# Kernel optimization log

Hardware: AMD Instinct MI355X
Metric: run time of the kernel (lower is better)

Reference implementation:

```python
import jax, jax.numpy as jnp
import numpy as np

N_NODES = 50000
N_EDGES = 1600000
D_FEAT = 32


def setup_inputs() -> dict:
    key = jax.random.key(0)
    k1, k2, k3, k4 = jax.random.split(key, 4)
    node_feat = jax.random.normal(k1, (N_NODES, D_FEAT), dtype=jnp.float32)
    edge_feat = jax.random.normal(k2, (N_EDGES, D_FEAT), dtype=jnp.float32)
    eps = jnp.zeros((1,), dtype=jnp.float32)  # learnable eps, init 0
    src = jax.random.randint(k3, (N_EDGES,), 0, N_NODES, dtype=jnp.int64)
    dst = jax.random.randint(k4, (N_EDGES,), 0, N_NODES, dtype=jnp.int64)
    return {"node_feat": node_feat, "edge_feat": edge_feat, "eps": eps,
            "src": src, "dst": dst}


def reference(node_feat, edge_feat, eps, src, dst):
    # message: relu(h_src + h_edge) per edge  [E, D]
    m = jax.nn.relu(node_feat[src] + edge_feat)
    # sum-aggregate messages into destination nodes  [N, D]
    neigh = jax.ops.segment_sum(m, dst, num_segments=node_feat.shape[0])
    # eps-scaled residual
    return (1.0 + eps[0]) * node_feat + neigh
```

## Files before the change

kernel.cpp:

```cpp
#include <hip/hip_runtime.h>

#define N_NODES 50000
#define N_EDGES 1600000
#define D_FEAT 32
#define SCAN_BLOCK 1024
#define N_SCAN_BLOCKS ((N_NODES + SCAN_BLOCK - 1) / SCAN_BLOCK)

#define WS_CNT   0
#define WS_EXCL  (N_NODES)
#define WS_OFF   (2 * N_NODES)
#define WS_BSUM  (3 * N_NODES)
#define WS_BSUMX (3 * N_NODES + 64)
#define WS_RANK  (3 * N_NODES + 128)
#define WS_MSG   (3 * N_NODES + 128 + N_EDGES)


__global__ void hist_rank(const int* __restrict__ dst,
                          int* __restrict__ cnt,
                          int* __restrict__ rank) {
    int e = blockIdx.x * blockDim.x + threadIdx.x;
    if (e < N_EDGES) rank[e] = atomicAdd(&cnt[dst[e]], 1);
}

__global__ void scan_blocks(const int* __restrict__ cnt,
                            int* __restrict__ excl,
                            int* __restrict__ bsum) {
    __shared__ int lds[SCAN_BLOCK];
    int tid = threadIdx.x;
    int i = blockIdx.x * SCAN_BLOCK + tid;
    int v = (i < N_NODES) ? cnt[i] : 0;
    int sum = v;
    lds[tid] = v;
    __syncthreads();
    for (int ofs = 1; ofs < SCAN_BLOCK; ofs <<= 1) {
        int t = (tid >= ofs) ? lds[tid - ofs] : 0;
        __syncthreads();
        sum += t;
        lds[tid] = sum;
        __syncthreads();
    }
    if (i < N_NODES) excl[i] = sum - v;
    if (tid == SCAN_BLOCK - 1) bsum[blockIdx.x] = lds[SCAN_BLOCK - 1];
}

__global__ void scan_bsums(const int* __restrict__ bsum, int* __restrict__ bsumx) {
    int lane = threadIdx.x;
    int orig = (lane < N_SCAN_BLOCKS) ? bsum[lane] : 0;
    int v = orig;
    for (int o = 1; o < 64; o <<= 1) {
        int t = __shfl_up(v, o);
        if (lane >= o) v += t;
    }
    if (lane < N_SCAN_BLOCKS) bsumx[lane] = v - orig;
}

__global__ void finalize_off(const int* __restrict__ excl,
                             const int* __restrict__ bsumx,
                             int* __restrict__ off) {
    int i = blockIdx.x * SCAN_BLOCK + threadIdx.x;
    if (i < N_NODES) off[i] = excl[i] + bsumx[blockIdx.x];
}

__global__ void build_msg(const float* __restrict__ node_feat,
                          const float* __restrict__ edge_feat,
                          const int* __restrict__ src,
                          const int* __restrict__ dst,
                          const int* __restrict__ off,
                          const int* __restrict__ rank,
                          float* __restrict__ msg) {
    int t = blockIdx.x * blockDim.x + threadIdx.x;
    int e = t >> 3;
    int g = t & 7;
    if (e >= N_EDGES) return;

    int d = dst[e];
    int pos = off[d] + rank[e];
    int s = src[e];

    float4 ef = ((const float4*)edge_feat)[(size_t)e * 8 + g];
    float4 nf = ((const float4*)node_feat)[s * 8 + g];
    float4 m;
    m.x = fmaxf(nf.x + ef.x, 0.f);
    m.y = fmaxf(nf.y + ef.y, 0.f);
    m.z = fmaxf(nf.z + ef.z, 0.f);
    m.w = fmaxf(nf.w + ef.w, 0.f);
    ((float4*)msg)[(size_t)pos * 8 + g] = m;
}

__global__ void reduce_msgs(const float* __restrict__ node_feat,
                            const float* __restrict__ eps,
                            const int* __restrict__ off,
                            const int* __restrict__ cnt,
                            const float* __restrict__ msg,
                            float* __restrict__ out) {
    int t = blockIdx.x * blockDim.x + threadIdx.x;
    int n = t >> 3;
    int g = t & 7;
    if (n >= N_NODES) return;

    int start = off[n];
    int c = cnt[n];

    float4 acc = make_float4(0.f, 0.f, 0.f, 0.f);
    for (int i = 0; i < c; ++i) {
        float4 m = ((const float4*)msg)[(size_t)(start + i) * 8 + g];
        acc.x += m.x; acc.y += m.y; acc.z += m.z; acc.w += m.w;
    }

    float scale = 1.0f + eps[0];
    float4 h = ((const float4*)node_feat)[n * 8 + g];
    float4 o;
    o.x = scale * h.x + acc.x;
    o.y = scale * h.y + acc.y;
    o.z = scale * h.z + acc.z;
    o.w = scale * h.w + acc.w;
    ((float4*)out)[n * 8 + g] = o;
}


__global__ void fb_init_out(const float* __restrict__ node_feat,
                            const float* __restrict__ eps,
                            float* __restrict__ out) {
    int i = blockIdx.x * blockDim.x + threadIdx.x;
    const int n4 = N_NODES * D_FEAT / 4;
    float scale = 1.0f + eps[0];
    if (i < n4) {
        float4 v = ((const float4*)node_feat)[i];
        v.x *= scale; v.y *= scale; v.z *= scale; v.w *= scale;
        ((float4*)out)[i] = v;
    }
}

__global__ void fb_scatter(const float* __restrict__ node_feat,
                           const float* __restrict__ edge_feat,
                           const int* __restrict__ src,
                           const int* __restrict__ dst,
                           float* __restrict__ out) {
    int t = blockIdx.x * blockDim.x + threadIdx.x;
    int e = t >> 3;
    int g = t & 7;
    if (e >= N_EDGES) return;
    int s = src[e];
    int d = dst[e];
    float4 nf = ((const float4*)node_feat)[s * 8 + g];
    float4 ef = ((const float4*)edge_feat)[(size_t)e * 8 + g];
    float* op = out + (size_t)d * D_FEAT + g * 4;
    unsafeAtomicAdd(op + 0, fmaxf(nf.x + ef.x, 0.f));
    unsafeAtomicAdd(op + 1, fmaxf(nf.y + ef.y, 0.f));
    unsafeAtomicAdd(op + 2, fmaxf(nf.z + ef.z, 0.f));
    unsafeAtomicAdd(op + 3, fmaxf(nf.w + ef.w, 0.f));
}

extern "C" void kernel_launch(void* const* d_in, const int* in_sizes, int n_in,
                              void* d_out, int out_size, void* d_ws, size_t ws_size,
                              hipStream_t stream) {
    const float* node_feat = (const float*)d_in[0];
    const float* edge_feat = (const float*)d_in[1];
    const float* eps       = (const float*)d_in[2];
    const int*   src       = (const int*)d_in[3];
    const int*   dst       = (const int*)d_in[4];
    float* out = (float*)d_out;

    const int B = 256;
    const size_t need = ((size_t)WS_MSG + (size_t)N_EDGES * D_FEAT) * sizeof(int);

    if (ws_size < need) {
        int n4 = N_NODES * D_FEAT / 4;
        fb_init_out<<<(n4 + B - 1) / B, B, 0, stream>>>(node_feat, eps, out);
        long long total = (long long)N_EDGES * 8;
        fb_scatter<<<(int)((total + B - 1) / B), B, 0, stream>>>(
            node_feat, edge_feat, src, dst, out);
        return;
    }

    int* ws = (int*)d_ws;
    int*   cnt   = ws + WS_CNT;
    int*   excl  = ws + WS_EXCL;
    int*   off   = ws + WS_OFF;
    int*   bsum  = ws + WS_BSUM;
    int*   bsumx = ws + WS_BSUMX;
    int*   rank  = ws + WS_RANK;
    float* msg   = (float*)(ws + WS_MSG);

    hipMemsetAsync(cnt, 0, N_NODES * sizeof(int), stream);

    hist_rank<<<(N_EDGES + B - 1) / B, B, 0, stream>>>(dst, cnt, rank);
    scan_blocks<<<N_SCAN_BLOCKS, SCAN_BLOCK, 0, stream>>>(cnt, excl, bsum);
    scan_bsums<<<1, 64, 0, stream>>>(bsum, bsumx);
    finalize_off<<<N_SCAN_BLOCKS, SCAN_BLOCK, 0, stream>>>(excl, bsumx, off);

    long long etotal = (long long)N_EDGES * 8;
    build_msg<<<(int)((etotal + B - 1) / B), B, 0, stream>>>(
        node_feat, edge_feat, src, dst, off, rank, msg);

    long long ntotal = (long long)N_NODES * 8;
    reduce_msgs<<<(int)((ntotal + B - 1) / B), B, 0, stream>>>(
        node_feat, eps, off, cnt, msg, out);
}
```

Before: 508.6 us.

## Store intermediate messages as bf16 and fuse prefix scan into one kernel

Messages written to the CSR-sorted staging buffer are now rounded to bf16 and packed, which halves the intermediate write and read traffic between the build and reduce kernels. The three-kernel offset scan is replaced by a single-block scan where each thread sums a contiguous chunk, removing two launches and the extra excl/bsum buffers. The trade-off is lower precision in the summed messages, which could exceed tolerance, and a single-block scan that does strided uncoalesced reads.

```diff
diff --git a/kernel.cpp b/kernel.cpp
--- a/kernel.cpp
+++ b/kernel.cpp
@@ -3,17 +3,21 @@
 #define N_NODES 50000
 #define N_EDGES 1600000
 #define D_FEAT 32
-#define SCAN_BLOCK 1024
-#define N_SCAN_BLOCKS ((N_NODES + SCAN_BLOCK - 1) / SCAN_BLOCK)
+#define SCAN_THREADS 1024
 
 #define WS_CNT   0
-#define WS_EXCL  (N_NODES)
-#define WS_OFF   (2 * N_NODES)
-#define WS_BSUM  (3 * N_NODES)
-#define WS_BSUMX (3 * N_NODES + 64)
-#define WS_RANK  (3 * N_NODES + 128)
-#define WS_MSG   (3 * N_NODES + 128 + N_EDGES)
+#define WS_OFF   (N_NODES)
+#define WS_RANK  (2 * N_NODES)
+#define WS_MSG   (2 * N_NODES + N_EDGES)
 
+static __device__ __forceinline__ unsigned short f2bf(float f) {
+    unsigned u = __float_as_uint(f);
+    unsigned r = (u + 0x7FFFu + ((u >> 16) & 1u)) >> 16;
+    return (unsigned short)r;
+}
+static __device__ __forceinline__ float bf2f(unsigned short h) {
+    return __uint_as_float(((unsigned)h) << 16);
+}
 
 __global__ void hist_rank(const int* __restrict__ dst,
                           int* __restrict__ cnt,
@@ -22,52 +26,38 @@
     if (e < N_EDGES) rank[e] = atomicAdd(&cnt[dst[e]], 1);
 }
 
-__global__ void scan_blocks(const int* __restrict__ cnt,
-                            int* __restrict__ excl,
-                            int* __restrict__ bsum) {
-    __shared__ int lds[SCAN_BLOCK];
-    int tid = threadIdx.x;
-    int i = blockIdx.x * SCAN_BLOCK + tid;
-    int v = (i < N_NODES) ? cnt[i] : 0;
-    int sum = v;
-    lds[tid] = v;
+__global__ void scan_all(const int* __restrict__ cnt, int* __restrict__ off) {
+    __shared__ int part[SCAN_THREADS];
+    const int PER = (N_NODES + SCAN_THREADS - 1) / SCAN_THREADS;
+    int t = threadIdx.x;
+    int base = t * PER;
+    int s = 0;
+    for (int i = 0; i < PER; ++i) {
+        int idx = base + i;
+        if (idx < N_NODES) s += cnt[idx];
+    }
+    part[t] = s;
     __syncthreads();
-    for (int ofs = 1; ofs < SCAN_BLOCK; ofs <<= 1) {
-        int t = (tid >= ofs) ? lds[tid - ofs] : 0;
+    for (int o = 1; o < SCAN_THREADS; o <<= 1) {
+        int v = (t >= o) ? part[t - o] : 0;
         __syncthreads();
-        sum += t;
-        lds[tid] = sum;
+        part[t] += v;
         __syncthreads();
     }
-    if (i < N_NODES) excl[i] = sum - v;
-    if (tid == SCAN_BLOCK - 1) bsum[blockIdx.x] = lds[SCAN_BLOCK - 1];
+    int run = (t > 0) ? part[t - 1] : 0;
+    for (int i = 0; i < PER; ++i) {
+        int idx = base + i;
+        if (idx < N_NODES) { off[idx] = run; run += cnt[idx]; }
+    }
 }
 
-__global__ void scan_bsums(const int* __restrict__ bsum, int* __restrict__ bsumx) {
-    int lane = threadIdx.x;
-    int orig = (lane < N_SCAN_BLOCKS) ? bsum[lane] : 0;
-    int v = orig;
-    for (int o = 1; o < 64; o <<= 1) {
-        int t = __shfl_up(v, o);
-        if (lane >= o) v += t;
-    }
-    if (lane < N_SCAN_BLOCKS) bsumx[lane] = v - orig;
-}
-
-__global__ void finalize_off(const int* __restrict__ excl,
-                             const int* __restrict__ bsumx,
-                             int* __restrict__ off) {
-    int i = blockIdx.x * SCAN_BLOCK + threadIdx.x;
-    if (i < N_NODES) off[i] = excl[i] + bsumx[blockIdx.x];
-}
-
-__global__ void build_msg(const float* __restrict__ node_feat,
-                          const float* __restrict__ edge_feat,
-                          const int* __restrict__ src,
-                          const int* __restrict__ dst,
-                          const int* __restrict__ off,
-                          const int* __restrict__ rank,
-                          float* __restrict__ msg) {
+__global__ void build_msg_bf16(const float* __restrict__ node_feat,
+                               const float* __restrict__ edge_feat,
+                               const int* __restrict__ src,
+                               const int* __restrict__ dst,
+                               const int* __restrict__ off,
+                               const int* __restrict__ rank,
+                               unsigned int* __restrict__ msg) {
     int t = blockIdx.x * blockDim.x + threadIdx.x;
     int e = t >> 3;
     int g = t & 7;
@@ -79,19 +69,22 @@
 
     float4 ef = ((const float4*)edge_feat)[(size_t)e * 8 + g];
     float4 nf = ((const float4*)node_feat)[s * 8 + g];
-    float4 m;
-    m.x = fmaxf(nf.x + ef.x, 0.f);
-    m.y = fmaxf(nf.y + ef.y, 0.f);
-    m.z = fmaxf(nf.z + ef.z, 0.f);
-    m.w = fmaxf(nf.w + ef.w, 0.f);
-    ((float4*)msg)[(size_t)pos * 8 + g] = m;
+    float m0 = fmaxf(nf.x + ef.x, 0.f);
+    float m1 = fmaxf(nf.y + ef.y, 0.f);
+    float m2 = fmaxf(nf.z + ef.z, 0.f);
+    float m3 = fmaxf(nf.w + ef.w, 0.f);
+
+    uint2 packed;
+    packed.x = (unsigned)f2bf(m0) | ((unsigned)f2bf(m1) << 16);
+    packed.y = (unsigned)f2bf(m2) | ((unsigned)f2bf(m3) << 16);
+    ((uint2*)msg)[(size_t)pos * 8 + g] = packed;
 }
 
 __global__ void reduce_msgs(const float* __restrict__ node_feat,
                             const float* __restrict__ eps,
                             const int* __restrict__ off,
                             const int* __restrict__ cnt,
-                            const float* __restrict__ msg,
+                            const unsigned int* __restrict__ msg,
                             float* __restrict__ out) {
     int t = blockIdx.x * blockDim.x + threadIdx.x;
     int n = t >> 3;
@@ -103,8 +96,11 @@
 
     float4 acc = make_float4(0.f, 0.f, 0.f, 0.f);
     for (int i = 0; i < c; ++i) {
-        float4 m = ((const float4*)msg)[(size_t)(start + i) * 8 + g];
-        acc.x += m.x; acc.y += m.y; acc.z += m.z; acc.w += m.w;
+        uint2 m = ((const uint2*)msg)[(size_t)(start + i) * 8 + g];
+        acc.x += bf2f((unsigned short)(m.x & 0xFFFF));
+        acc.y += bf2f((unsigned short)(m.x >> 16));
+        acc.z += bf2f((unsigned short)(m.y & 0xFFFF));
+        acc.w += bf2f((unsigned short)(m.y >> 16));
     }
 
     float scale = 1.0f + eps[0];
@@ -162,7 +158,7 @@
     float* out = (float*)d_out;
 
     const int B = 256;
-    const size_t need = ((size_t)WS_MSG + (size_t)N_EDGES * D_FEAT) * sizeof(int);
+    const size_t need = (size_t)WS_MSG * sizeof(int) + (size_t)N_EDGES * 64;
 
     if (ws_size < need) {
         int n4 = N_NODES * D_FEAT / 4;
@@ -174,23 +170,18 @@
     }
 
     int* ws = (int*)d_ws;
-    int*   cnt   = ws + WS_CNT;
-    int*   excl  = ws + WS_EXCL;
-    int*   off   = ws + WS_OFF;
-    int*   bsum  = ws + WS_BSUM;
-    int*   bsumx = ws + WS_BSUMX;
-    int*   rank  = ws + WS_RANK;
-    float* msg   = (float*)(ws + WS_MSG);
+    int*          cnt  = ws + WS_CNT;
+    int*          off  = ws + WS_OFF;
+    int*          rank = ws + WS_RANK;
+    unsigned int* msg  = (unsigned int*)(ws + WS_MSG);
 
     hipMemsetAsync(cnt, 0, N_NODES * sizeof(int), stream);
 
     hist_rank<<<(N_EDGES + B - 1) / B, B, 0, stream>>>(dst, cnt, rank);
-    scan_blocks<<<N_SCAN_BLOCKS, SCAN_BLOCK, 0, stream>>>(cnt, excl, bsum);
-    scan_bsums<<<1, 64, 0, stream>>>(bsum, bsumx);
-    finalize_off<<<N_SCAN_BLOCKS, SCAN_BLOCK, 0, stream>>>(excl, bsumx, off);
+    scan_all<<<1, SCAN_THREADS, 0, stream>>>(cnt, off);
 
     long long etotal = (long long)N_EDGES * 8;
-    build_msg<<<(int)((etotal + B - 1) / B), B, 0, stream>>>(
+    build_msg_bf16<<<(int)((etotal + B - 1) / B), B, 0, stream>>>(
         node_feat, edge_feat, src, dst, off, rank, msg);
 
     long long ntotal = (long long)N_NODES * 8;
```

New measurement: 522.6 us. +2.8%, slower.
